# Kernel optimization log

Hardware: AMD Instinct MI355X
Metric: run time of the kernel (lower is better)

## Reference

```python
import jax, jax.numpy as jnp
import numpy as np

H, HKV, D, HID, INT = 16, 4, 128, 2048, 8192
ROPE_THETA = 10000.0
EPS = 1e-6
NEG = -1e30


def rmsnorm(x, w):
    v = jnp.mean(x * x, axis=-1, keepdims=True)
    return x * jax.lax.rsqrt(v + EPS) * w


def apply_rope(t, pos):
    # t: [B,S,h,D], pos: [S]
    half = D // 2
    inv_freq = 1.0 / (ROPE_THETA ** (jnp.arange(0, half, dtype=jnp.float32) / half))
    ang = pos.astype(jnp.float32)[:, None] * inv_freq  # [S, D/2]
    cos = jnp.cos(ang)[None, :, None, :]
    sin = jnp.sin(ang)[None, :, None, :]
    t1, t2 = t[..., :half], t[..., half:]
    return jnp.concatenate([t1 * cos - t2 * sin, t2 * cos + t1 * sin], axis=-1)


def setup_inputs() -> dict:
    key = jax.random.key(0)
    ks = jax.random.split(key, 5)
    B, S = 4, 1024
    s = 0.02  # init scale for weights
    return {
        "x": jax.random.normal(ks[0], (B, S, HID), jnp.float32),
        "ln1_w": jnp.ones((HID,), jnp.float32),
        "wqkv": jax.random.normal(ks[1], (HID, (H + 2 * HKV) * D), jnp.float32) * s,
        "wo": jax.random.normal(ks[2], (H * D, HID), jnp.float32) * s,
        "ln2_w": jnp.ones((HID,), jnp.float32),
        "w_gate_up": jax.random.normal(ks[3], (HID, 2 * INT), jnp.float32) * s,
        "w_down": jax.random.normal(ks[4], (INT, HID), jnp.float32) * s,
        "pos": jnp.arange(S, dtype=jnp.int32),
    }


def reference(x, ln1_w, wqkv, wo, ln2_w, w_gate_up, w_down, pos):
    B, S, _ = x.shape
    # --- attention block (prefill paged attention == dense causal attention) ---
    h = rmsnorm(x, ln1_w)
    qkv = h @ wqkv  # [B,S,(H+2*HKV)*D]
    q = qkv[..., : H * D].reshape(B, S, H, D)
    k = qkv[..., H * D : (H + HKV) * D].reshape(B, S, HKV, D)
    v = qkv[..., (H + HKV) * D :].reshape(B, S, HKV, D)
    q = apply_rope(q, pos)
    k = apply_rope(k, pos)
    g = H // HKV  # GQA group size
    k = jnp.repeat(k, g, axis=2)
    v = jnp.repeat(v, g, axis=2)
    scores = jnp.einsum("bqhd,bkhd->bhqk", q, k) / np.float32(np.sqrt(D))
    causal = pos[:, None] >= pos[None, :]  # [S,S]
    scores = jnp.where(causal[None, None], scores, NEG)
    attn = jax.nn.softmax(scores, axis=-1)
    o = jnp.einsum("bhqk,bkhd->bqhd", attn, v).reshape(B, S, H * D) @ wo
    h1 = x + o
    # --- SwiGLU MLP block ---
    gu = rmsnorm(h1, ln2_w) @ w_gate_up
    gate, up = gu[..., :INT], gu[..., INT:]
    return h1 + (jax.nn.silu(gate) * up) @ w_down
```

## Files before the change

kernel.cpp:

```cpp
#include <hip/hip_runtime.h>
#include <math.h>

#define B_    4
#define S_    1024
#define H_    16
#define HKV_  4
#define D_    128
#define HID_  2048
#define INT_  8192
#define QKVD_ 3072
#define NTOK_ 4096
#define NEG_  -1.0e30f

typedef unsigned short u16;
typedef unsigned int   u32;
typedef float  f32x4  __attribute__((ext_vector_type(4)));
typedef __bf16 bf16x8 __attribute__((ext_vector_type(8)));

__device__ __forceinline__ float bf2f(u16 v) {
    union { u32 u; float f; } c; c.u = ((u32)v) << 16; return c.f;
}
__device__ __forceinline__ u16 f2bf(float f) {
    union { float f; u32 u; } c; c.f = f;
    return (u16)((c.u + 0x7fffu + ((c.u >> 16) & 1u)) >> 16);
}

__device__ __forceinline__ void async_ld16(const u16* g, u16* l) {
    __builtin_amdgcn_global_load_lds(
        (const __attribute__((address_space(1))) void*)g,
        (__attribute__((address_space(3))) void*)l, 16, 0, 0);
}

__global__ void detect_k(const u16* __restrict__ w, int* __restrict__ flag) {
    if (threadIdx.x == 0) *flag = (w[0] == 0x3F80u) ? 0 : 1;
}

__global__ void cvt_x_k(const void* __restrict__ in, const int* __restrict__ flag,
                        u16* __restrict__ out) {
    int i = blockIdx.x * 256 + threadIdx.x;
    if (*flag == 0) {
        ((ushort4*)out)[i] = ((const ushort4*)in)[i];
    } else {
        float4 v = ((const float4*)in)[i];
        ushort4 o;
        o.x = f2bf(v.x); o.y = f2bf(v.y); o.z = f2bf(v.z); o.w = f2bf(v.w);
        ((ushort4*)out)[i] = o;
    }
}

__global__ void cvt_w_k(const void* __restrict__ in, const int* __restrict__ flag,
                        float* __restrict__ out, int n) {
    int i = blockIdx.x * 256 + threadIdx.x;
    if (i < n) out[i] = (*flag == 0) ? bf2f(((const u16*)in)[i]) : ((const float*)in)[i];
}

__global__ void transpose_k(const void* __restrict__ in, const int* __restrict__ flag,
                            u16* __restrict__ out, int K, int N) {
    __shared__ u16 t[64][65];
    const bool isf32 = (*flag != 0);
    int tx = blockIdx.x * 64;
    int ty = blockIdx.y * 64;
    const int c4 = (threadIdx.x & 15) * 4;
    const int r0 = threadIdx.x >> 4;
    for (int r = r0; r < 64; r += 16) {
        size_t idx = (size_t)(ty + r) * N + tx + c4;
        if (isf32) {
            float4 v = *(const float4*)((const float*)in + idx);
            t[c4 + 0][r] = f2bf(v.x); t[c4 + 1][r] = f2bf(v.y);
            t[c4 + 2][r] = f2bf(v.z); t[c4 + 3][r] = f2bf(v.w);
        } else {
            ushort4 v = *(const ushort4*)((const u16*)in + idx);
            t[c4 + 0][r] = v.x; t[c4 + 1][r] = v.y;
            t[c4 + 2][r] = v.z; t[c4 + 3][r] = v.w;
        }
    }
    __syncthreads();
    for (int i = threadIdx.x; i < 64 * 16; i += 256) {
        int r = i >> 4, c = (i & 15) * 4;
        ushort4 v;
        v.x = t[r][c]; v.y = t[r][c + 1]; v.z = t[r][c + 2]; v.w = t[r][c + 3];
        *(ushort4*)(out + (size_t)(tx + r) * K + ty + c) = v;
    }
}

__global__ void rmsnorm_k(const u16* __restrict__ x, const float* __restrict__ w,
                          u16* __restrict__ y) {
    int row = blockIdx.x;
    const u16* xr = x + (size_t)row * HID_;
    u16* yr = y + (size_t)row * HID_;
    int t = threadIdx.x;
    u16 xs[8];
    *(uint4*)xs = ((const uint4*)xr)[t];
    float v[8]; float ss = 0.f;
    #pragma unroll
    for (int i = 0; i < 8; i++) { v[i] = bf2f(xs[i]); ss += v[i] * v[i]; }
    #pragma unroll
    for (int o = 32; o > 0; o >>= 1) ss += __shfl_down(ss, o, 64);
    __shared__ float wsum[4];
    if ((t & 63) == 0) wsum[t >> 6] = ss;
    __syncthreads();
    float tot = wsum[0] + wsum[1] + wsum[2] + wsum[3];
    float scale = rsqrtf(tot * (1.0f / HID_) + 1e-6f);
    float4 w0 = ((const float4*)w)[t * 2];
    float4 w1 = ((const float4*)w)[t * 2 + 1];
    float wf[8] = {w0.x, w0.y, w0.z, w0.w, w1.x, w1.y, w1.z, w1.w};
    u16 ys[8];
    #pragma unroll
    for (int i = 0; i < 8; i++) ys[i] = f2bf(v[i] * scale * wf[i]);
    ((uint4*)yr)[t] = *(uint4*)ys;
}

__global__ void rope_table_k(const int* __restrict__ pos,
                             float* __restrict__ cosT, float* __restrict__ sinT) {
    int s = blockIdx.x;
    int d = threadIdx.x;
    double inv = exp(-((double)d / 64.0) * 9.210340371976184);
    double ang = (double)pos[s] * inv;
    cosT[s * 64 + d] = (float)cos(ang);
    sinT[s * 64 + d] = (float)sin(ang);
}

__global__ void rope_apply_k(u16* __restrict__ qkv, const float* __restrict__ cosT,
                             const float* __restrict__ sinT) {
    int id = blockIdx.x * 256 + threadIdx.x;
    int d4 = (id & 15) * 4;
    int rest = id >> 4;
    int head = rest % 20;
    int bs = rest / 20;
    int s = bs & (S_ - 1);
    size_t base = (size_t)bs * QKVD_ + head * D_;
    ushort4 lo = *(ushort4*)(qkv + base + d4);
    ushort4 hi = *(ushort4*)(qkv + base + 64 + d4);
    float4 c  = *(const float4*)(cosT + s * 64 + d4);
    float4 sn = *(const float4*)(sinT + s * 64 + d4);
    float t1[4] = {bf2f(lo.x), bf2f(lo.y), bf2f(lo.z), bf2f(lo.w)};
    float t2[4] = {bf2f(hi.x), bf2f(hi.y), bf2f(hi.z), bf2f(hi.w)};
    float cf[4] = {c.x, c.y, c.z, c.w};
    float sf[4] = {sn.x, sn.y, sn.z, sn.w};
    ushort4 olo, ohi;
    olo.x = f2bf(t1[0] * cf[0] - t2[0] * sf[0]);
    olo.y = f2bf(t1[1] * cf[1] - t2[1] * sf[1]);
    olo.z = f2bf(t1[2] * cf[2] - t2[2] * sf[2]);
    olo.w = f2bf(t1[3] * cf[3] - t2[3] * sf[3]);
    ohi.x = f2bf(t2[0] * cf[0] + t1[0] * sf[0]);
    ohi.y = f2bf(t2[1] * cf[1] + t1[1] * sf[1]);
    ohi.z = f2bf(t2[2] * cf[2] + t1[2] * sf[2]);
    ohi.w = f2bf(t2[3] * cf[3] + t1[3] * sf[3]);
    *(ushort4*)(qkv + base + d4)      = olo;
    *(ushort4*)(qkv + base + 64 + d4) = ohi;
}

template<int EPI>
__global__ __launch_bounds__(256) void gemm_bt_k(
    const u16* __restrict__ A, const u16* __restrict__ Bt,
    void* __restrict__ Cv, const u16* __restrict__ R,
    const int* __restrict__ flag, int M, int N, int K)
{
    __shared__ __align__(16) u16 As[128 * 32];
    __shared__ __align__(16) u16 Bs[128 * 32];

    int bx = blockIdx.x, by = blockIdx.y;
    {
        const int gx  = gridDim.x;
        const int nwg = gx * gridDim.y;
        const int orig = by * gx + bx;
        const int q = nwg >> 3, r = nwg & 7;
        const int xcd = orig & 7, loc = orig >> 3;
        const int wg = (xcd < r ? xcd * (q + 1) : r * (q + 1) + (xcd - r) * q) + loc;
        bx = wg % gx; by = wg / gx;
    }

    const int tid  = threadIdx.x;
    const int m0 = by * 128;
    const int n0 = bx * 128;
    const int wave = tid >> 6, lane = tid & 63;
    const int wm = (wave & 1) * 64, wn = (wave >> 1) * 64;
    const int r16 = lane & 15, quad = lane >> 4;

    const int f0 = tid * 8;
    const int f1 = f0 + 2048;
    const size_t arow0 = (size_t)(m0 + (f0 >> 5)) * K + (f0 & 31);
    const size_t arow1 = (size_t)(m0 + (f1 >> 5)) * K + (f1 & 31);
    const size_t brow0 = (size_t)(n0 + (f0 >> 5)) * K + (f0 & 31);
    const size_t brow1 = (size_t)(n0 + (f1 >> 5)) * K + (f1 & 31);

    f32x4 acc[4][4] = {};

    for (int k0 = 0; k0 < K; k0 += 32) {
        async_ld16(A  + arow0 + k0, As + f0);
        async_ld16(A  + arow1 + k0, As + f1);
        async_ld16(Bt + brow0 + k0, Bs + f0);
        async_ld16(Bt + brow1 + k0, Bs + f1);
        __syncthreads();
        bf16x8 a[4], b[4];
        #pragma unroll
        for (int i = 0; i < 4; i++)
            a[i] = *(const bf16x8*)(As + (wm + i * 16 + r16) * 32 + quad * 8);
        #pragma unroll
        for (int j = 0; j < 4; j++)
            b[j] = *(const bf16x8*)(Bs + (wn + j * 16 + r16) * 32 + quad * 8);
        #pragma unroll
        for (int i = 0; i < 4; i++)
            #pragma unroll
            for (int j = 0; j < 4; j++)
                acc[i][j] = __builtin_amdgcn_mfma_f32_16x16x32_bf16(a[i], b[j], acc[i][j], 0, 0, 0);
        __syncthreads();
    }

    u16* C16 = (u16*)Cv;
    float* C32 = (float*)Cv;
    bool f32out = false;
    if (EPI == 3) f32out = (*flag != 0);

    #pragma unroll
    for (int i = 0; i < 4; i++) {
        const int mb = m0 + wm + i * 16 + quad * 4;
        #pragma unroll
        for (int j = 0; j < 4; j++) {
            const int n = n0 + wn + j * 16 + r16;
            #pragma unroll
            for (int r = 0; r < 4; r++) {
                size_t idx = (size_t)(mb + r) * N + n;
                float v = acc[i][j][r];
                if (EPI == 1 || EPI == 3) v += bf2f(R[idx]);
                if (EPI == 2) { v = v / (1.f + __expf(-v)); v *= bf2f(C16[idx]); }
                if (EPI == 3 && f32out) C32[idx] = v;
                else C16[idx] = f2bf(v);
            }
        }
    }
}

__global__ __launch_bounds__(256) void attn_mfma_k(
    const u16* __restrict__ qkv, u16* __restrict__ out)
{
    __shared__ __align__(16) u16 Vt[128 * 136];
    __shared__ __align__(16) u16 Ps[64 * 136];

    int bswz_x, bswz_y, bswz_z;
    {
        const int nwg = (S_ / 64) * H_ * B_;
        const int orig = blockIdx.x + (S_ / 64) * (blockIdx.y + H_ * blockIdx.z);
        const int q = nwg >> 3;
        const int wg = (orig & 7) * q + (orig >> 3);
        bswz_x = wg & (S_ / 64 - 1);
        bswz_y = (wg >> 4) & (H_ - 1);
        bswz_z = wg >> 8;
    }

    const int tid  = threadIdx.x;
    const int wave = tid >> 6, lane = tid & 63;
    const int r16  = lane & 15, quad = lane >> 4;
    const int q0 = bswz_x * 64;
    const int h  = bswz_y;
    const int b  = bswz_z;
    const int kh = h >> 2;
    const float scale = 0.08838834764831845f;

    bf16x8 a_q[4];
    {
        const u16* qp = qkv + ((size_t)(b * S_ + q0 + wave * 16 + r16) * QKVD_ + h * D_ + quad * 8);
        #pragma unroll
        for (int ks = 0; ks < 4; ks++)
            a_q[ks] = *(const bf16x8*)(qp + ks * 32);
    }

    float mrun[4], lrun[4];
    #pragma unroll
    for (int r = 0; r < 4; r++) { mrun[r] = -3.0e38f; lrun[r] = 0.f; }
    f32x4 acc_o[8] = {};
    const int myrow_c = q0 + wave * 16 + quad * 4;

    const int ntiles = (q0 >> 7) + 1;
    for (int kt = 0; kt < ntiles; kt++) {
        const int j0 = kt * 128;
        __syncthreads();
        {
            const int key = tid & 127, dh = (tid >> 7) * 64;
            const u16* vp = qkv + ((size_t)(b * S_ + j0 + key) * QKVD_ + (H_ + HKV_ + kh) * D_ + dh);
            #pragma unroll
            for (int i = 0; i < 8; i++) {
                u16 tmp[8];
                *(uint4*)tmp = *(const uint4*)(vp + i * 8);
                #pragma unroll
                for (int j = 0; j < 8; j++)
                    Vt[(dh + i * 8 + j) * 136 + key] = tmp[j];
            }
        }
        f32x4 acc_s[8] = {};
        __builtin_amdgcn_s_setprio(1);
        #pragma unroll
        for (int ks = 0; ks < 4; ks++) {
            #pragma unroll
            for (int nt = 0; nt < 8; nt++) {
                const u16* kp = qkv + ((size_t)(b * S_ + j0 + nt * 16 + r16) * QKVD_
                                       + (H_ + kh) * D_ + ks * 32 + quad * 8);
                bf16x8 bk = *(const bf16x8*)kp;
                acc_s[nt] = __builtin_amdgcn_mfma_f32_16x16x32_bf16(a_q[ks], bk, acc_s[nt], 0, 0, 0);
            }
        }
        __builtin_amdgcn_s_setprio(0);
        const bool lastt = (kt == ntiles - 1);
        float mnew[4];
        #pragma unroll
        for (int r = 0; r < 4; r++) mnew[r] = mrun[r];
        #pragma unroll
        for (int nt = 0; nt < 8; nt++) {
            const int col = j0 + nt * 16 + r16;
            #pragma unroll
            for (int r = 0; r < 4; r++) {
                float v = acc_s[nt][r] * scale;
                if (lastt && col > myrow_c + r) v = NEG_;
                acc_s[nt][r] = v;
                mnew[r] = fmaxf(mnew[r], v);
            }
        }
        #pragma unroll
        for (int o = 1; o < 16; o <<= 1)
            #pragma unroll
            for (int r = 0; r < 4; r++)
                mnew[r] = fmaxf(mnew[r], __shfl_xor(mnew[r], o, 64));
        float alpha[4], lsum[4];
        #pragma unroll
        for (int r = 0; r < 4; r++) {
            alpha[r] = __expf(mrun[r] - mnew[r]);
            mrun[r] = mnew[r];
            lsum[r] = 0.f;
        }
        #pragma unroll
        for (int nt = 0; nt < 8; nt++) {
            #pragma unroll
            for (int r = 0; r < 4; r++) {
                float p = __expf(acc_s[nt][r] - mrun[r]);
                lsum[r] += p;
                Ps[(wave * 16 + quad * 4 + r) * 136 + nt * 16 + r16] = f2bf(p);
            }
        }
        #pragma unroll
        for (int o = 1; o < 16; o <<= 1)
            #pragma unroll
            for (int r = 0; r < 4; r++)
                lsum[r] += __shfl_xor(lsum[r], o, 64);
        #pragma unroll
        for (int r = 0; r < 4; r++) lrun[r] = lrun[r] * alpha[r] + lsum[r];
        #pragma unroll
        for (int nt = 0; nt < 8; nt++)
            #pragma unroll
            for (int r = 0; r < 4; r++) acc_o[nt][r] *= alpha[r];
        __syncthreads();
        __builtin_amdgcn_s_setprio(1);
        #pragma unroll
        for (int ks = 0; ks < 4; ks++) {
            bf16x8 ap = *(const bf16x8*)(Ps + (wave * 16 + r16) * 136 + ks * 32 + quad * 8);
            #pragma unroll
            for (int nt = 0; nt < 8; nt++) {
                bf16x8 bv = *(const bf16x8*)(Vt + (nt * 16 + r16) * 136 + ks * 32 + quad * 8);
                acc_o[nt] = __builtin_amdgcn_mfma_f32_16x16x32_bf16(ap, bv, acc_o[nt], 0, 0, 0);
            }
        }
        __builtin_amdgcn_s_setprio(0);
    }
    #pragma unroll
    for (int r = 0; r < 4; r++) {
        const float linv = 1.0f / lrun[r];
        const int tok = myrow_c + r;
        u16* orow = out + ((size_t)(b * S_ + tok) * (H_ * D_) + h * D_ + r16);
        #pragma unroll
        for (int nt = 0; nt < 8; nt++)
            orow[nt * 16] = f2bf(acc_o[nt][r] * linv);
    }
}

extern "C" void kernel_launch(void* const* d_in, const int* in_sizes, int n_in,
                              void* d_out, int out_size, void* d_ws, size_t ws_size,
                              hipStream_t stream)
{
    const void* x    = d_in[0];
    const u16*  ln1w = (const u16*)d_in[1];
    const void* wqkv = d_in[2];
    const void* wo   = d_in[3];
    const void* ln2w = d_in[4];
    const void* wgu  = d_in[5];
    const void* wd   = d_in[6];
    const int*  pos  = (const int*)d_in[7];

    char* wsb = (char*)d_ws;
    size_t off = 0;
    auto alloc = [&](size_t bytes) {
        char* p = wsb + off; off = (off + bytes + 255) & ~(size_t)255; return p;
    };
    int*  flag  = (int*)alloc(256);
    u16*  xb    = (u16*)alloc(2ull * NTOK_ * HID_);
    float* wln1 = (float*)alloc(4ull * HID_);
    float* wln2 = (float*)alloc(4ull * HID_);
    u16* wqkvT = (u16*)alloc(2ull * 3072 * 2048);
    u16* woT   = (u16*)alloc(2ull * 2048 * 2048);
    u16* wguT  = (u16*)alloc(2ull * 16384 * 2048);
    u16* wdT   = (u16*)alloc(2ull * 2048 * 8192);
    u16* h     = (u16*)alloc(2ull * NTOK_ * HID_);
    u16* qkv   = (u16*)alloc(2ull * NTOK_ * QKVD_);
    u16* h1    = (u16*)alloc(2ull * NTOK_ * HID_);
    u16* su    = (u16*)alloc(2ull * NTOK_ * INT_);
    float* cosT = (float*)alloc(4ull * S_ * 64);
    float* sinT = (float*)alloc(4ull * S_ * 64);
    u16* attn_out = h;
    u16* mlp_in   = qkv;

    detect_k<<<1, 64, 0, stream>>>(ln1w, flag);

    cvt_x_k<<<(NTOK_ * HID_ / 4 + 255) / 256, 256, 0, stream>>>(x, flag, xb);
    cvt_w_k<<<8, 256, 0, stream>>>(d_in[1], flag, wln1, HID_);
    cvt_w_k<<<8, 256, 0, stream>>>(ln2w, flag, wln2, HID_);

    transpose_k<<<dim3(3072 / 64, 2048 / 64), 256, 0, stream>>>(wqkv, flag, wqkvT, 2048, 3072);
    transpose_k<<<dim3(2048 / 64, 2048 / 64), 256, 0, stream>>>(wo, flag, woT, 2048, 2048);
    transpose_k<<<dim3(16384 / 64, 2048 / 64), 256, 0, stream>>>(wgu, flag, wguT, 2048, 16384);
    transpose_k<<<dim3(2048 / 64, 8192 / 64), 256, 0, stream>>>(wd, flag, wdT, 8192, 2048);

    rope_table_k<<<S_, 64, 0, stream>>>(pos, cosT, sinT);

    rmsnorm_k<<<NTOK_, 256, 0, stream>>>(xb, wln1, h);
    gemm_bt_k<0><<<dim3(3072 / 128, NTOK_ / 128), 256, 0, stream>>>(
        h, wqkvT, qkv, nullptr, nullptr, NTOK_, QKVD_, HID_);
    rope_apply_k<<<(NTOK_ * 20 * 16) / 256, 256, 0, stream>>>(qkv, cosT, sinT);
    attn_mfma_k<<<dim3(S_ / 64, H_, B_), 256, 0, stream>>>(qkv, attn_out);
    gemm_bt_k<1><<<dim3(2048 / 128, NTOK_ / 128), 256, 0, stream>>>(
        attn_out, woT, h1, xb, nullptr, NTOK_, HID_, HID_);
    rmsnorm_k<<<NTOK_, 256, 0, stream>>>(h1, wln2, mlp_in);
    gemm_bt_k<0><<<dim3(8192 / 128, NTOK_ / 128), 256, 0, stream>>>(
        mlp_in, wguT + (size_t)8192 * 2048, su, nullptr, nullptr, NTOK_, INT_, HID_);
    gemm_bt_k<2><<<dim3(8192 / 128, NTOK_ / 128), 256, 0, stream>>>(
        mlp_in, wguT, su, nullptr, nullptr, NTOK_, INT_, HID_);
    gemm_bt_k<3><<<dim3(2048 / 128, NTOK_ / 128), 256, 0, stream>>>(
        su, wdT, d_out, h1, flag, NTOK_, HID_, INT_);
}
```

Measured before the change: 1.254 ms.

## Add 256x256-tile triple-buffered GEMM kernel for QKV and gate/up projections

Introduces a new 512-thread GEMM kernel with 256x256 output tiles, triple-buffered async LDS staging, split A/B prefetch interleaved with two MFMA phases, and priority hints around the MFMA bursts. It replaces the 128x128 kernel for the QKV projection and both gate/up projections. The goal is more data reuse per tile and more overlap of loads with MFMA work. In exchange the kernel uses a large accumulator register file and large LDS buffers, which may limit occupancy, and the QKV launch has only 192 workgroups.

```diff
diff --git a/kernel.cpp b/kernel.cpp
--- a/kernel.cpp
+++ b/kernel.cpp
@@ -223,9 +223,120 @@
                 size_t idx = (size_t)(mb + r) * N + n;
                 float v = acc[i][j][r];
                 if (EPI == 1 || EPI == 3) v += bf2f(R[idx]);
-                if (EPI == 2) { v = v / (1.f + __expf(-v)); v *= bf2f(C16[idx]); }
                 if (EPI == 3 && f32out) C32[idx] = v;
                 else C16[idx] = f2bf(v);
+            }
+        }
+    }
+}
+
+template<int EPI>
+__global__ __launch_bounds__(512, 2) void gemm256_k(
+    const u16* __restrict__ A, const u16* __restrict__ Bt,
+    void* __restrict__ Cv, int M, int N, int K)
+{
+    __shared__ __align__(16) u16 lds[3 * 16384];
+
+    int bx = blockIdx.x, by = blockIdx.y;
+    {
+        const int gx  = gridDim.x;
+        const int nwg = gx * gridDim.y;
+        const int orig = by * gx + bx;
+        const int q = nwg >> 3, r = nwg & 7;
+        const int xcd = orig & 7, loc = orig >> 3;
+        const int wg = (xcd < r ? xcd * (q + 1) : r * (q + 1) + (xcd - r) * q) + loc;
+        bx = wg % gx; by = wg / gx;
+    }
+
+    const int tid  = threadIdx.x;
+    const int m0 = by * 256, n0 = bx * 256;
+    const int wave = tid >> 6, lane = tid & 63;
+    const int wmi = wave >> 2, wni = wave & 3;
+    const int r16 = lane & 15, quad = lane >> 4;
+
+    const int NT = K >> 5;
+
+    auto stageA = [&](int bufi, int tt) {
+        u16* dst = lds + bufi * 16384;
+        const size_t gb = (size_t)m0 * K + (size_t)tt * 32;
+        #pragma unroll
+        for (int rr = 0; rr < 2; ++rr) {
+            const int e = rr * 4096 + tid * 8;
+            async_ld16(A + gb + (size_t)(e >> 5) * K + (e & 31), dst + e);
+        }
+    };
+    auto stageB = [&](int bufi, int tt) {
+        u16* dst = lds + bufi * 16384 + 8192;
+        const size_t gb = (size_t)n0 * K + (size_t)tt * 32;
+        #pragma unroll
+        for (int rr = 0; rr < 2; ++rr) {
+            const int e = rr * 4096 + tid * 8;
+            async_ld16(Bt + gb + (size_t)(e >> 5) * K + (e & 31), dst + e);
+        }
+    };
+
+    f32x4 acc[8][4] = {};
+
+    stageA(0, 0); stageB(0, 0);
+    stageA(1, 1); stageB(1, 1);
+    asm volatile("s_waitcnt vmcnt(4)" ::: "memory");
+    __builtin_amdgcn_s_barrier();
+
+    const int aoff = wmi * 4096 + r16 * 32 + quad * 8;
+    const int boff = 8192 + wni * 2048 + r16 * 32 + quad * 8;
+
+    for (int t = 0; t < NT; ++t) {
+        const u16* buf = lds + (t % 3) * 16384;
+        const int nb = (t + 2) % 3;
+        const bool pf = (t + 2) < NT;
+        bf16x8 a[4], b[4], a2[4];
+        #pragma unroll
+        for (int i = 0; i < 4; ++i) a[i] = *(const bf16x8*)(buf + aoff + i * 512);
+        #pragma unroll
+        for (int j = 0; j < 4; ++j) b[j] = *(const bf16x8*)(buf + boff + j * 512);
+        if (pf) stageA(nb, t + 2);
+        __builtin_amdgcn_s_barrier();
+        asm volatile("s_waitcnt lgkmcnt(0)" ::: "memory");
+        __builtin_amdgcn_sched_barrier(0);
+        __builtin_amdgcn_s_setprio(1);
+        #pragma unroll
+        for (int i = 0; i < 4; ++i)
+            #pragma unroll
+            for (int j = 0; j < 4; ++j)
+                acc[i][j] = __builtin_amdgcn_mfma_f32_16x16x32_bf16(a[i], b[j], acc[i][j], 0, 0, 0);
+        __builtin_amdgcn_s_setprio(0);
+        __builtin_amdgcn_s_barrier();
+        #pragma unroll
+        for (int i = 0; i < 4; ++i) a2[i] = *(const bf16x8*)(buf + aoff + (i + 4) * 512);
+        if (pf) stageB(nb, t + 2);
+        __builtin_amdgcn_s_barrier();
+        asm volatile("s_waitcnt lgkmcnt(0)" ::: "memory");
+        __builtin_amdgcn_sched_barrier(0);
+        __builtin_amdgcn_s_setprio(1);
+        #pragma unroll
+        for (int i = 0; i < 4; ++i)
+            #pragma unroll
+            for (int j = 0; j < 4; ++j)
+                acc[i + 4][j] = __builtin_amdgcn_mfma_f32_16x16x32_bf16(a2[i], b[j], acc[i + 4][j], 0, 0, 0);
+        __builtin_amdgcn_s_setprio(0);
+        if (t == NT - 2) { asm volatile("s_waitcnt vmcnt(0)" ::: "memory"); }
+        else             { asm volatile("s_waitcnt vmcnt(4)" ::: "memory"); }
+        __builtin_amdgcn_s_barrier();
+    }
+
+    u16* C16 = (u16*)Cv;
+    #pragma unroll
+    for (int i = 0; i < 8; ++i) {
+        const int mb = m0 + wmi * 128 + i * 16 + quad * 4;
+        #pragma unroll
+        for (int j = 0; j < 4; ++j) {
+            const int n = n0 + wni * 64 + j * 16 + r16;
+            #pragma unroll
+            for (int r = 0; r < 4; ++r) {
+                size_t idx = (size_t)(mb + r) * N + n;
+                float v = acc[i][j][r];
+                if (EPI == 2) { v = v / (1.f + __expf(-v)); v *= bf2f(C16[idx]); }
+                C16[idx] = f2bf(v);
             }
         }
     }
@@ -239,9 +350,8 @@
 
     int bswz_x, bswz_y, bswz_z;
     {
-        const int nwg = (S_ / 64) * H_ * B_;
         const int orig = blockIdx.x + (S_ / 64) * (blockIdx.y + H_ * blockIdx.z);
-        const int q = nwg >> 3;
+        const int q = ((S_ / 64) * H_ * B_) >> 3;
         const int wg = (orig & 7) * q + (orig >> 3);
         bswz_x = wg & (S_ / 64 - 1);
         bswz_y = (wg >> 4) & (H_ - 1);
@@ -420,17 +530,17 @@
     rope_table_k<<<S_, 64, 0, stream>>>(pos, cosT, sinT);
 
     rmsnorm_k<<<NTOK_, 256, 0, stream>>>(xb, wln1, h);
-    gemm_bt_k<0><<<dim3(3072 / 128, NTOK_ / 128), 256, 0, stream>>>(
-        h, wqkvT, qkv, nullptr, nullptr, NTOK_, QKVD_, HID_);
+    gemm256_k<0><<<dim3(3072 / 256, NTOK_ / 256), 512, 0, stream>>>(
+        h, wqkvT, qkv, NTOK_, QKVD_, HID_);
     rope_apply_k<<<(NTOK_ * 20 * 16) / 256, 256, 0, stream>>>(qkv, cosT, sinT);
     attn_mfma_k<<<dim3(S_ / 64, H_, B_), 256, 0, stream>>>(qkv, attn_out);
     gemm_bt_k<1><<<dim3(2048 / 128, NTOK_ / 128), 256, 0, stream>>>(
         attn_out, woT, h1, xb, nullptr, NTOK_, HID_, HID_);
     rmsnorm_k<<<NTOK_, 256, 0, stream>>>(h1, wln2, mlp_in);
-    gemm_bt_k<0><<<dim3(8192 / 128, NTOK_ / 128), 256, 0, stream>>>(
-        mlp_in, wguT + (size_t)8192 * 2048, su, nullptr, nullptr, NTOK_, INT_, HID_);
-    gemm_bt_k<2><<<dim3(8192 / 128, NTOK_ / 128), 256, 0, stream>>>(
-        mlp_in, wguT, su, nullptr, nullptr, NTOK_, INT_, HID_);
+    gemm256_k<0><<<dim3(8192 / 256, NTOK_ / 256), 512, 0, stream>>>(
+        mlp_in, wguT + (size_t)8192 * 2048, su, NTOK_, INT_, HID_);
+    gemm256_k<2><<<dim3(8192 / 256, NTOK_ / 256), 512, 0, stream>>>(
+        mlp_in, wguT, su, NTOK_, INT_, HID_);
     gemm_bt_k<3><<<dim3(2048 / 128, NTOK_ / 128), 256, 0, stream>>>(
         su, wdT, d_out, h1, flag, NTOK_, HID_, INT_);
 }
```

New measurement: 1.150 ms. 8.3% less time.
